# Optimization experiments

Measured on AMD Instinct MI355X. Metric: run time of the kernel, lower is better.

The kernel has to match this reference:

```python
import jax, jax.numpy as jnp
import numpy as np

N = 50000
E = 1_600_000
IN_C = 128
OUT_C = 128


def _glorot(key, shape):
    fan_in, fan_out = shape[0], shape[1]
    s = jnp.sqrt(6.0 / (fan_in + fan_out))
    return jax.random.uniform(key, shape, jnp.float32, -s, s)


def setup_inputs() -> dict:
    key = jax.random.key(0)
    ks = jax.random.split(key, 32)
    inp = {
        'X': jax.random.normal(ks[0], (N, IN_C), jnp.float32),
        'edge_index': jax.random.randint(ks[1], (2, E), 0, N, jnp.int64),
        'edge_weight': jax.random.uniform(ks[2], (E,), jnp.float32),
        'H': jax.random.normal(ks[3], (N, OUT_C), jnp.float32),
        'C': jax.random.normal(ks[4], (N, OUT_C), jnp.float32),
    }
    i = 5
    for g in ('i', 'f', 'c', 'o'):
        inp[f'Wx_{g}'] = _glorot(ks[i], (IN_C, OUT_C)); i += 1
        inp[f'bx_{g}'] = jnp.zeros((OUT_C,), jnp.float32)
        inp[f'Wh_{g}'] = _glorot(ks[i], (OUT_C, OUT_C)); i += 1
        inp[f'bh_{g}'] = jnp.zeros((OUT_C,), jnp.float32)
    for g in ('i', 'f', 'o'):
        inp[f'w_c_{g}'] = _glorot(ks[i], (1, OUT_C)); i += 1
    for g in ('i', 'f', 'c', 'o'):
        inp[f'b_{g}'] = jnp.zeros((1, OUT_C), jnp.float32)
    return inp


def reference(X, edge_index, edge_weight, H, C,
              Wx_i, bx_i, Wh_i, bh_i,
              Wx_f, bx_f, Wh_f, bh_f,
              Wx_c, bx_c, Wh_c, bh_c,
              Wx_o, bx_o, Wh_o, bh_o,
              w_c_i, w_c_f, w_c_o,
              b_i, b_f, b_c, b_o):
    n = X.shape[0]
    src, dst = edge_index[0], edge_index[1]
    # GCN normalization (add_self_loops=False): deg from destination (in-degree)
    deg = jax.ops.segment_sum(edge_weight, dst, num_segments=n)
    dis = jnp.where(deg > 0, jax.lax.rsqrt(jnp.where(deg > 0, deg, 1.0)), 0.0)
    norm = dis[src] * edge_weight * dis[dst]  # [E]

    def gcn(x, W, b):
        xw = x @ W                       # [n, OUT_C]
        msg = xw[src] * norm[:, None]    # gather + scale, [E, OUT_C]
        return jax.ops.segment_sum(msg, dst, num_segments=n) + b

    I = jax.nn.sigmoid(gcn(X, Wx_i, bx_i) + gcn(H, Wh_i, bh_i) + w_c_i * C + b_i)
    Fg = jax.nn.sigmoid(gcn(X, Wx_f, bx_f) + gcn(H, Wh_f, bh_f) + w_c_f * C + b_f)
    T = jnp.tanh(gcn(X, Wx_c, bx_c) + gcn(H, Wh_c, bh_c) + b_c)
    Cn = Fg * C + I * T
    O = jax.nn.sigmoid(gcn(X, Wx_o, bx_o) + gcn(H, Wh_o, bh_o) + w_c_o * Cn + b_o)
    Hn = O * jnp.tanh(Cn)
    return Hn, Cn
```

## Files before the change

### kernel.cpp

```cpp
#include <hip/hip_runtime.h>

__device__ __forceinline__ float bf2f(unsigned short u){
    union { unsigned int i; float f; } v; v.i = ((unsigned int)u) << 16; return v.f;
}
__device__ __forceinline__ unsigned short f2bf(float f){
    union { unsigned int i; float f; } v; v.f = f;
    unsigned int i = v.i;
    unsigned int r = i + 0x7FFFu + ((i >> 16) & 1u);
    return (unsigned short)(r >> 16);
}
__device__ __forceinline__ float sigm(float x){ return 1.0f / (1.0f + __expf(-x)); }

__device__ __forceinline__ float ldsel(const void* p, size_t idx, int fF){
    float r;
    if (fF) r = ((const float*)p)[idx];
    else    r = bf2f(((const unsigned short*)p)[idx]);
    return r;
}

typedef __attribute__((ext_vector_type(8))) short s8v;
typedef __attribute__((ext_vector_type(4))) float f4v;

__global__ void k_detect(const unsigned short* __restrict__ X,
                         const int* __restrict__ ei, int* __restrict__ flags){
    __shared__ int cnt, nz;
    if (threadIdx.x == 0){ cnt = 0; nz = 0; }
    __syncthreads();
    int ok = 0;
    for (int i = threadIdx.x; i < 2048; i += 256){
        int e = (X[i] >> 7) & 0xFF;
        if (e >= 96 && e <= 160) ok++;
    }
    atomicAdd(&cnt, ok);
    int nzl = 0;
    for (int i = threadIdx.x; i < 128; i += 256)
        if (ei[2*i + 1] != 0) nzl++;
    atomicAdd(&nz, nzl);
    __syncthreads();
    if (threadIdx.x == 0){
        flags[0] = (cnt < 1843) ? 1 : 0;
        flags[1] = (nz == 0)   ? 1 : 0;
    }
}

struct PackArgs {
    const void* Wx[4];
    const void* Wh[4];
    const void* bx[4];
    const void* bh[4];
};

__global__ void k_tobf(const void* __restrict__ X, const void* __restrict__ H,
                       uint4* __restrict__ XHb128, const int* __restrict__ flags,
                       int N){
    int t = blockIdx.x*256 + threadIdx.x;
    if (t >= N*32) return;
    int n = t >> 5, i = t & 31;
    int fF = flags[0];
    int q = (i < 16) ? i : i - 16;
    uint4 o;
    if (fF){
        const float4* src = (const float4*)((i < 16) ? X : H);
        float4 a = src[(size_t)n*32 + q*2];
        float4 b = src[(size_t)n*32 + q*2 + 1];
        o.x = ((unsigned int)f2bf(a.y) << 16) | f2bf(a.x);
        o.y = ((unsigned int)f2bf(a.w) << 16) | f2bf(a.z);
        o.z = ((unsigned int)f2bf(b.y) << 16) | f2bf(b.x);
        o.w = ((unsigned int)f2bf(b.w) << 16) | f2bf(b.z);
    } else {
        const uint4* src = (const uint4*)((i < 16) ? X : H);
        o = src[(size_t)n*16 + q];
    }
    XHb128[(size_t)n*32 + i] = o;
}

__global__ void k_cnt(const int* __restrict__ ei, int* __restrict__ cnt,
                      int* __restrict__ off, const int* __restrict__ flags,
                      int E, int N){
    int base = blockIdx.x*1024 + threadIdx.x;
    int fI = flags[1];
#pragma unroll
    for (int k = 0; k < 4; k++){
        int e = base + k*256;
        if (e >= E) break;
        int d = fI ? ei[2*(size_t)E + 2*(size_t)e] : ei[(size_t)E + e];
        if ((unsigned)d >= (unsigned)N) continue;
        off[e] = atomicAdd(&cnt[d], 1);
    }
}

__global__ void k_pack(PackArgs pa, unsigned short* __restrict__ Bp,
                       float* __restrict__ bias, const int* __restrict__ flags){
    int t = blockIdx.x*256 + threadIdx.x;
    int fF = flags[0];
    {
        int j    =  t        & 7;
        int lane = (t >> 3)  & 63;
        int kb   = (t >> 9)  & 7;
        int ct   = (t >> 12) & 7;
        int g    = (t >> 15) & 3;
        int k   = kb*32 + (lane >> 4)*8 + j;
        int col = ct*16 + (lane & 15);
        const void* p; size_t idx;
        if (k < 128){ p = pa.Wx[g]; idx = (size_t)k*128 + col; }
        else        { p = pa.Wh[g]; idx = (size_t)(k-128)*128 + col; }
        unsigned short v;
        if (fF) v = f2bf(((const float*)p)[idx]);
        else    v = ((const unsigned short*)p)[idx];
        Bp[t] = v;
    }
    if (t < 512){
        int g = t >> 7, c = t & 127;
        bias[t] = ldsel(pa.bx[g], c, fF) + ldsel(pa.bh[g], c, fF);
    }
}

__global__ void k_scanA(const int* __restrict__ cnt, int* __restrict__ bsum, int n){
    __shared__ int sh[256];
    int t = threadIdx.x, i = blockIdx.x * 256 + t;
    sh[t] = (i < n) ? cnt[i] : 0;
    __syncthreads();
    for (int o = 128; o > 0; o >>= 1){
        if (t < o) sh[t] += sh[t + o];
        __syncthreads();
    }
    if (t == 0) bsum[blockIdx.x] = sh[0];
}
__global__ void k_scanB(const int* __restrict__ bsum, int* __restrict__ bsumoff, int nb){
    __shared__ int sh[256];
    int t = threadIdx.x;
    int v = (t < nb) ? bsum[t] : 0;
    sh[t] = v;
    __syncthreads();
    for (int o = 1; o < 256; o <<= 1){
        int u = (t >= o) ? sh[t - o] : 0;
        __syncthreads();
        sh[t] += u;
        __syncthreads();
    }
    bsumoff[t] = sh[t] - v;
}
__global__ void k_scanC(const int* __restrict__ cnt, const int* __restrict__ bsumoff,
                        int* __restrict__ rowstart, int n){
    __shared__ int sh[256];
    int t = threadIdx.x, i = blockIdx.x * 256 + t;
    int v = (i < n) ? cnt[i] : 0;
    sh[t] = v;
    __syncthreads();
    for (int o = 1; o < 256; o <<= 1){
        int u = (t >= o) ? sh[t - o] : 0;
        __syncthreads();
        sh[t] += u;
        __syncthreads();
    }
    int incl = sh[t];
    if (i < n)     rowstart[i] = bsumoff[blockIdx.x] + incl - v;
    if (i == n-1)  rowstart[n] = bsumoff[blockIdx.x] + incl;
}

__global__ void k_scatter(const int* __restrict__ ei, const void* __restrict__ ew,
                          const int* __restrict__ rowstart, const int* __restrict__ off,
                          int2* __restrict__ recs, const int* __restrict__ flags,
                          int E, int N){
    int base = blockIdx.x*512 + threadIdx.x;
    int fF = flags[0], fI = flags[1];
#pragma unroll
    for (int k = 0; k < 2; k++){
        int e = base + k*256;
        if (e >= E) break;
        int s, d;
        if (fI){ s = ei[2*(size_t)e]; d = ei[2*(size_t)E + 2*(size_t)e]; }
        else   { s = ei[e];           d = ei[(size_t)E + e]; }
        if ((unsigned)d >= (unsigned)N) continue;
        float w = 0.f; int ss = 0;
        if ((unsigned)s < (unsigned)N){ w = ldsel(ew, e, fF); ss = s; }
        int2 r; r.x = ss; r.y = __float_as_int(w);
        recs[rowstart[d] + off[e]] = r;
    }
}

__global__ __launch_bounds__(256)
void k_degdis(const int2* __restrict__ recs, const int* __restrict__ rowstart,
              float* __restrict__ dis, int N){
    int gw = (blockIdx.x * 256 + threadIdx.x) >> 6;
    int lane = threadIdx.x & 63;
    if (gw >= N) return;
    int beg = rowstart[gw], end = rowstart[gw + 1];
    float sw = 0.f;
    for (int i = beg + lane; i < end; i += 64) sw += __int_as_float(recs[i].y);
    for (int o = 32; o > 0; o >>= 1) sw += __shfl_down(sw, o);
    if (lane == 0) dis[gw] = (sw > 0.f) ? rsqrtf(sw) : 0.f;
}

__global__ __launch_bounds__(256)
void k_gather(const int2* __restrict__ recs, const int* __restrict__ rowstart,
              const float* __restrict__ dis, const uint4* __restrict__ XHb128,
              uint4* __restrict__ AXH128, int N){
    int node = (blockIdx.x * 256 + threadIdx.x) >> 6;
    int lane = threadIdx.x & 63;
    if (node >= N) return;
    int half = lane >> 5;
    int sub  = lane & 31;
    int beg = rowstart[node], end = rowstart[node + 1];
    float disd = dis[node];
    float a0=0.f,a1=0.f,a2=0.f,a3=0.f,a4=0.f,a5=0.f,a6=0.f,a7=0.f;

#define ACC8(v, n)                                              \
    a0 += (n) * bf2f((unsigned short)((v).x & 0xffff));         \
    a1 += (n) * bf2f((unsigned short)((v).x >> 16));            \
    a2 += (n) * bf2f((unsigned short)((v).y & 0xffff));         \
    a3 += (n) * bf2f((unsigned short)((v).y >> 16));            \
    a4 += (n) * bf2f((unsigned short)((v).z & 0xffff));         \
    a5 += (n) * bf2f((unsigned short)((v).z >> 16));            \
    a6 += (n) * bf2f((unsigned short)((v).w & 0xffff));         \
    a7 += (n) * bf2f((unsigned short)((v).w >> 16));

    int i = beg;
    for (; i + 3 < end; i += 4){
        int2 rA = recs[i + half];
        int2 rB = recs[i + 2 + half];
        uint4 vA = XHb128[(size_t)rA.x*32 + sub];
        uint4 vB = XHb128[(size_t)rB.x*32 + sub];
        float nA = dis[rA.x] * __int_as_float(rA.y) * disd;
        float nB = dis[rB.x] * __int_as_float(rB.y) * disd;
        ACC8(vA, nA);
        ACC8(vB, nB);
    }
    if (end - i >= 2){
        int2 rA = recs[i + half];
        uint4 vA = XHb128[(size_t)rA.x*32 + sub];
        float nA = dis[rA.x] * __int_as_float(rA.y) * disd;
        ACC8(vA, nA);
        i += 2;
    }
    if (i < end){
        int2 rA = recs[i];
        uint4 vA = XHb128[(size_t)rA.x*32 + sub];
        float nA = (half == 0) ? dis[rA.x] * __int_as_float(rA.y) * disd : 0.f;
        ACC8(vA, nA);
    }
#undef ACC8

    a0 += __shfl_xor(a0, 32, 64);
    a1 += __shfl_xor(a1, 32, 64);
    a2 += __shfl_xor(a2, 32, 64);
    a3 += __shfl_xor(a3, 32, 64);
    a4 += __shfl_xor(a4, 32, 64);
    a5 += __shfl_xor(a5, 32, 64);
    a6 += __shfl_xor(a6, 32, 64);
    a7 += __shfl_xor(a7, 32, 64);

    if (half == 0){
        uint4 o;
        o.x = ((unsigned int)f2bf(a1) << 16) | f2bf(a0);
        o.y = ((unsigned int)f2bf(a3) << 16) | f2bf(a2);
        o.z = ((unsigned int)f2bf(a5) << 16) | f2bf(a4);
        o.w = ((unsigned int)f2bf(a7) << 16) | f2bf(a6);
        AXH128[(size_t)node*32 + sub] = o;
    }
}

struct EpiArgs {
    const void *C, *wci, *wcf, *wco, *bi, *bff, *bc, *bo;
};

__global__ __launch_bounds__(256)
void k_gemm(const unsigned short* __restrict__ AXH,
            const unsigned short* __restrict__ Bp, const float* __restrict__ bias,
            EpiArgs ea, void* __restrict__ outp, const int* __restrict__ flags, int N){
    int tid  = threadIdx.x;
    int w    = tid >> 6, lane = tid & 63;
    int node0 = blockIdx.x * 32;
    int fF = flags[0];

    f4v acc[2][8];
#pragma unroll
    for (int m = 0; m < 2; m++)
#pragma unroll
        for (int c = 0; c < 8; c++) acc[m][c] = (f4v){0.f,0.f,0.f,0.f};

    const unsigned short* a0base = AXH + (size_t)(node0 + (lane & 15))*256 + (lane >> 4)*8;
    const unsigned short* a1base = a0base + 16*256;
#pragma unroll
    for (int kb = 0; kb < 8; kb++){
        s8v af0 = *(const s8v*)(a0base + kb*32);
        s8v af1 = *(const s8v*)(a1base + kb*32);
#pragma unroll
        for (int ct8 = 0; ct8 < 8; ct8++){
            int g = ct8 >> 1, sub = ct8 & 1;
            const s8v bfrag = *(const s8v*)(Bp + g*32768 + (size_t)(w*2 + sub)*4096
                                            + kb*512 + lane*8);
            acc[0][ct8] = __builtin_amdgcn_mfma_f32_16x16x32_bf16(af0, bfrag, acc[0][ct8], 0, 0, 0);
            acc[1][ct8] = __builtin_amdgcn_mfma_f32_16x16x32_bf16(af1, bfrag, acc[1][ct8], 0, 0, 0);
        }
    }

    int q = lane >> 4, cl = lane & 15;
#pragma unroll
    for (int sub = 0; sub < 2; sub++){
        int c = w*32 + sub*16 + cl;
        float bvi = bias[0*128 + c], bvf = bias[1*128 + c];
        float bvc = bias[2*128 + c], bvo = bias[3*128 + c];
        float wci = ldsel(ea.wci, c, fF), wcf = ldsel(ea.wcf, c, fF), wco = ldsel(ea.wco, c, fF);
        float bi  = ldsel(ea.bi, c, fF),  bff = ldsel(ea.bff, c, fF);
        float bc  = ldsel(ea.bc, c, fF),  bo  = ldsel(ea.bo, c, fF);
#pragma unroll
        for (int m = 0; m < 2; m++){
#pragma unroll
            for (int r = 0; r < 4; r++){
                int node = node0 + m*16 + q*4 + r;
                if (node >= N) continue;
                size_t gidx = (size_t)node*128 + c;
                float Cv = ldsel(ea.C, gidx, fF);
                float pi  = acc[m][0+sub][r] + bvi;
                float pf  = acc[m][2+sub][r] + bvf;
                float pcv = acc[m][4+sub][r] + bvc;
                float po  = acc[m][6+sub][r] + bvo;
                float Iv = sigm(pi + wci*Cv + bi);
                float Fv = sigm(pf + wcf*Cv + bff);
                float Tv = tanhf(pcv + bc);
                float Cn = Fv*Cv + Iv*Tv;
                float Ov = sigm(po + wco*Cn + bo);
                float Hn = Ov * tanhf(Cn);
                if (fF){
                    ((float*)outp)[gidx] = Hn;
                    ((float*)outp)[(size_t)N*128 + gidx] = Cn;
                } else {
                    ((unsigned short*)outp)[gidx] = f2bf(Hn);
                    ((unsigned short*)outp)[(size_t)N*128 + gidx] = f2bf(Cn);
                }
            }
        }
    }
}

extern "C" void kernel_launch(void* const* d_in, const int* in_sizes, int n_in,
                              void* d_out, int out_size, void* d_ws, size_t ws_size,
                              hipStream_t stream){
    const void* X  = d_in[0];
    const int*  ei = (const int*)d_in[1];
    const void* ew = d_in[2];
    const void* H  = d_in[3];
    const void* C  = d_in[4];
    const int N = in_sizes[0] / 128;
    const int E = in_sizes[2];

    char* ws = (char*)d_ws;
    int*   cnt          = (int*)  (ws);
    float* dis          = (float*)(ws + ((size_t)256 << 10));
    int*   rowstart     = (int*)  (ws + ((size_t)512 << 10));
    int*   bsum         = (int*)  (ws + ((size_t)768 << 10));
    int*   bsumoff      = (int*)  (ws + ((size_t)772 << 10));
    int*   flags        = (int*)  (ws + ((size_t)776 << 10));
    unsigned short* Bp  = (unsigned short*)(ws + ((size_t)1 << 20));
    float* bias         = (float*)(ws + ((size_t)1 << 20) + ((size_t)256 << 10));
    int*   off          = (int*)  (ws + ((size_t)2 << 20));
    unsigned int* AXH32 = (unsigned int*)(ws + ((size_t)2 << 20));
    int2*  recs         = (int2*) (ws + ((size_t)28 << 20));
    unsigned int* XHb32 = (unsigned int*)(ws + ((size_t)41 << 20));

    hipMemsetAsync(cnt, 0, (size_t)256 << 10, stream);
    k_detect<<<1, 256, 0, stream>>>((const unsigned short*)X, ei, flags);

    PackArgs pa;
    pa.Wx[0]=d_in[5];  pa.bx[0]=d_in[6];  pa.Wh[0]=d_in[7];  pa.bh[0]=d_in[8];
    pa.Wx[1]=d_in[9];  pa.bx[1]=d_in[10]; pa.Wh[1]=d_in[11]; pa.bh[1]=d_in[12];
    pa.Wx[2]=d_in[13]; pa.bx[2]=d_in[14]; pa.Wh[2]=d_in[15]; pa.bh[2]=d_in[16];
    pa.Wx[3]=d_in[17]; pa.bx[3]=d_in[18]; pa.Wh[3]=d_in[19]; pa.bh[3]=d_in[20];

    k_cnt<<<(E + 1023)/1024, 256, 0, stream>>>(ei, cnt, off, flags, E, N);
    k_tobf<<<(N*32 + 255)/256, 256, 0, stream>>>(X, H, (uint4*)XHb32, flags, N);
    k_pack<<<512, 256, 0, stream>>>(pa, Bp, bias, flags);

    int nbA = (N + 255)/256;
    k_scanA<<<nbA, 256, 0, stream>>>(cnt, bsum, N);
    k_scanB<<<1, 256, 0, stream>>>(bsum, bsumoff, nbA);
    k_scanC<<<nbA, 256, 0, stream>>>(cnt, bsumoff, rowstart, N);

    k_scatter<<<(E + 511)/512, 256, 0, stream>>>(ei, ew, rowstart, off, recs, flags, E, N);
    k_degdis<<<(N*64 + 255)/256, 256, 0, stream>>>(recs, rowstart, dis, N);
    k_gather<<<(N*64 + 255)/256, 256, 0, stream>>>(recs, rowstart, dis,
                                                   (const uint4*)XHb32,
                                                   (uint4*)AXH32, N);

    EpiArgs ea;
    ea.C   = C;
    ea.wci = d_in[21];
    ea.wcf = d_in[22];
    ea.wco = d_in[23];
    ea.bi  = d_in[24];
    ea.bff = d_in[25];
    ea.bc  = d_in[26];
    ea.bo  = d_in[27];
    k_gemm<<<(N + 31)/32, 256, 0, stream>>>((const unsigned short*)AXH32, Bp, bias,
                                            ea, d_out, flags, N);
}
```

Before: 506.2 us.

## Fuse preprocessing kernels, compute degree with atomics, unroll gather deeper

The edge-count, bf16 conversion and weight-packing kernels are merged into one launch that branches on block index. The weighted in-degree is now accumulated with float atomics during counting, and the inverse square root is folded into the scan. That removes the separate per-node degree-reduction pass over the edge records. The scatter kernel batches four edges' loads per thread before storing, and the gather loop is unrolled to eight edges to keep more loads in flight. The trade-offs are extra float atomic traffic, a summation order that is no longer deterministic, and higher register pressure in the gather kernel.

```diff
diff --git a/kernel.cpp b/kernel.cpp
--- a/kernel.cpp
+++ b/kernel.cpp
@@ -50,68 +50,79 @@
     const void* bh[4];
 };
 
-__global__ void k_tobf(const void* __restrict__ X, const void* __restrict__ H,
-                       uint4* __restrict__ XHb128, const int* __restrict__ flags,
-                       int N){
-    int t = blockIdx.x*256 + threadIdx.x;
-    if (t >= N*32) return;
-    int n = t >> 5, i = t & 31;
+__global__ void k_fused1(const void* __restrict__ X, const void* __restrict__ H,
+                         uint4* __restrict__ XHb128,
+                         const int* __restrict__ ei, const void* __restrict__ ew,
+                         int* __restrict__ cnt, float* __restrict__ deg,
+                         int* __restrict__ off,
+                         PackArgs pa, unsigned short* __restrict__ Bp,
+                         float* __restrict__ bias,
+                         const int* __restrict__ flags,
+                         int nbC, int nbT, int E, int N){
+    int b = blockIdx.x;
     int fF = flags[0];
-    int q = (i < 16) ? i : i - 16;
-    uint4 o;
-    if (fF){
-        const float4* src = (const float4*)((i < 16) ? X : H);
-        float4 a = src[(size_t)n*32 + q*2];
-        float4 b = src[(size_t)n*32 + q*2 + 1];
-        o.x = ((unsigned int)f2bf(a.y) << 16) | f2bf(a.x);
-        o.y = ((unsigned int)f2bf(a.w) << 16) | f2bf(a.z);
-        o.z = ((unsigned int)f2bf(b.y) << 16) | f2bf(b.x);
-        o.w = ((unsigned int)f2bf(b.w) << 16) | f2bf(b.z);
+    if (b < nbC){
+        int base = b*2048 + threadIdx.x;
+        int fI = flags[1];
+        int dd[8]; float wv[8];
+#pragma unroll
+        for (int k = 0; k < 8; k++){
+            int e = base + k*256;
+            dd[k] = -1; wv[k] = 0.f;
+            if (e < E){
+                dd[k] = fI ? ei[2*(size_t)E + 2*(size_t)e] : ei[(size_t)E + e];
+                wv[k] = ldsel(ew, e, fF);
+            }
+        }
+#pragma unroll
+        for (int k = 0; k < 8; k++){
+            int e = base + k*256;
+            if (e < E && (unsigned)dd[k] < (unsigned)N){
+                off[e] = atomicAdd(&cnt[dd[k]], 1);
+                atomicAdd(&deg[dd[k]], wv[k]);
+            }
+        }
+    } else if (b < nbC + nbT){
+        int t = (b - nbC)*256 + threadIdx.x;
+        if (t >= N*32) return;
+        int n = t >> 5, i = t & 31;
+        int q = (i < 16) ? i : i - 16;
+        uint4 o;
+        if (fF){
+            const float4* src = (const float4*)((i < 16) ? X : H);
+            float4 a = src[(size_t)n*32 + q*2];
+            float4 bb = src[(size_t)n*32 + q*2 + 1];
+            o.x = ((unsigned int)f2bf(a.y) << 16) | f2bf(a.x);
+            o.y = ((unsigned int)f2bf(a.w) << 16) | f2bf(a.z);
+            o.z = ((unsigned int)f2bf(bb.y) << 16) | f2bf(bb.x);
+            o.w = ((unsigned int)f2bf(bb.w) << 16) | f2bf(bb.z);
+        } else {
+            const uint4* src = (const uint4*)((i < 16) ? X : H);
+            o = src[(size_t)n*16 + q];
+        }
+        XHb128[(size_t)n*32 + i] = o;
     } else {
-        const uint4* src = (const uint4*)((i < 16) ? X : H);
-        o = src[(size_t)n*16 + q];
-    }
-    XHb128[(size_t)n*32 + i] = o;
-}
-
-__global__ void k_cnt(const int* __restrict__ ei, int* __restrict__ cnt,
-                      int* __restrict__ off, const int* __restrict__ flags,
-                      int E, int N){
-    int base = blockIdx.x*1024 + threadIdx.x;
-    int fI = flags[1];
-#pragma unroll
-    for (int k = 0; k < 4; k++){
-        int e = base + k*256;
-        if (e >= E) break;
-        int d = fI ? ei[2*(size_t)E + 2*(size_t)e] : ei[(size_t)E + e];
-        if ((unsigned)d >= (unsigned)N) continue;
-        off[e] = atomicAdd(&cnt[d], 1);
-    }
-}
-
-__global__ void k_pack(PackArgs pa, unsigned short* __restrict__ Bp,
-                       float* __restrict__ bias, const int* __restrict__ flags){
-    int t = blockIdx.x*256 + threadIdx.x;
-    int fF = flags[0];
-    {
-        int j    =  t        & 7;
-        int lane = (t >> 3)  & 63;
-        int kb   = (t >> 9)  & 7;
-        int ct   = (t >> 12) & 7;
-        int g    = (t >> 15) & 3;
-        int k   = kb*32 + (lane >> 4)*8 + j;
-        int col = ct*16 + (lane & 15);
-        const void* p; size_t idx;
-        if (k < 128){ p = pa.Wx[g]; idx = (size_t)k*128 + col; }
-        else        { p = pa.Wh[g]; idx = (size_t)(k-128)*128 + col; }
-        unsigned short v;
-        if (fF) v = f2bf(((const float*)p)[idx]);
-        else    v = ((const unsigned short*)p)[idx];
-        Bp[t] = v;
-    }
-    if (t < 512){
-        int g = t >> 7, c = t & 127;
-        bias[t] = ldsel(pa.bx[g], c, fF) + ldsel(pa.bh[g], c, fF);
+        int t = (b - nbC - nbT)*256 + threadIdx.x;
+        if (t < 4*8*8*64*8){
+            int j    =  t        & 7;
+            int lane = (t >> 3)  & 63;
+            int kb   = (t >> 9)  & 7;
+            int ct   = (t >> 12) & 7;
+            int g    = (t >> 15) & 3;
+            int k   = kb*32 + (lane >> 4)*8 + j;
+            int col = ct*16 + (lane & 15);
+            const void* p; size_t idx;
+            if (k < 128){ p = pa.Wx[g]; idx = (size_t)k*128 + col; }
+            else        { p = pa.Wh[g]; idx = (size_t)(k-128)*128 + col; }
+            unsigned short v;
+            if (fF) v = f2bf(((const float*)p)[idx]);
+            else    v = ((const unsigned short*)p)[idx];
+            Bp[t] = v;
+        }
+        if (t < 512){
+            int g = t >> 7, c = t & 127;
+            bias[t] = ldsel(pa.bx[g], c, fF) + ldsel(pa.bh[g], c, fF);
+        }
     }
 }
 
@@ -141,7 +152,8 @@
     bsumoff[t] = sh[t] - v;
 }
 __global__ void k_scanC(const int* __restrict__ cnt, const int* __restrict__ bsumoff,
-                        int* __restrict__ rowstart, int n){
+                        const float* __restrict__ deg,
+                        int* __restrict__ rowstart, float* __restrict__ dis, int n){
     __shared__ int sh[256];
     int t = threadIdx.x, i = blockIdx.x * 256 + t;
     int v = (i < n) ? cnt[i] : 0;
@@ -154,7 +166,11 @@
         __syncthreads();
     }
     int incl = sh[t];
-    if (i < n)     rowstart[i] = bsumoff[blockIdx.x] + incl - v;
+    if (i < n){
+        rowstart[i] = bsumoff[blockIdx.x] + incl - v;
+        float dg = deg[i];
+        dis[i] = (dg > 0.f) ? rsqrtf(dg) : 0.f;
+    }
     if (i == n-1)  rowstart[n] = bsumoff[blockIdx.x] + incl;
 }
 
@@ -162,34 +178,28 @@
                           const int* __restrict__ rowstart, const int* __restrict__ off,
                           int2* __restrict__ recs, const int* __restrict__ flags,
                           int E, int N){
-    int base = blockIdx.x*512 + threadIdx.x;
+    int base = blockIdx.x*1024 + threadIdx.x;
     int fF = flags[0], fI = flags[1];
-#pragma unroll
-    for (int k = 0; k < 2; k++){
+    int ss[4], dd[4], oo[4]; float wv[4];
+#pragma unroll
+    for (int k = 0; k < 4; k++){
         int e = base + k*256;
-        if (e >= E) break;
-        int s, d;
-        if (fI){ s = ei[2*(size_t)e]; d = ei[2*(size_t)E + 2*(size_t)e]; }
-        else   { s = ei[e];           d = ei[(size_t)E + e]; }
-        if ((unsigned)d >= (unsigned)N) continue;
-        float w = 0.f; int ss = 0;
-        if ((unsigned)s < (unsigned)N){ w = ldsel(ew, e, fF); ss = s; }
-        int2 r; r.x = ss; r.y = __float_as_int(w);
-        recs[rowstart[d] + off[e]] = r;
-    }
-}
-
-__global__ __launch_bounds__(256)
-void k_degdis(const int2* __restrict__ recs, const int* __restrict__ rowstart,
-              float* __restrict__ dis, int N){
-    int gw = (blockIdx.x * 256 + threadIdx.x) >> 6;
-    int lane = threadIdx.x & 63;
-    if (gw >= N) return;
-    int beg = rowstart[gw], end = rowstart[gw + 1];
-    float sw = 0.f;
-    for (int i = beg + lane; i < end; i += 64) sw += __int_as_float(recs[i].y);
-    for (int o = 32; o > 0; o >>= 1) sw += __shfl_down(sw, o);
-    if (lane == 0) dis[gw] = (sw > 0.f) ? rsqrtf(sw) : 0.f;
+        dd[k] = -1; ss[k] = 0; wv[k] = 0.f; oo[k] = 0;
+        if (e < E){
+            if (fI){ ss[k] = ei[2*(size_t)e]; dd[k] = ei[2*(size_t)E + 2*(size_t)e]; }
+            else   { ss[k] = ei[e];           dd[k] = ei[(size_t)E + e]; }
+            oo[k] = off[e];
+            if ((unsigned)ss[k] < (unsigned)N) wv[k] = ldsel(ew, e, fF);
+            else ss[k] = 0;
+        }
+    }
+#pragma unroll
+    for (int k = 0; k < 4; k++){
+        if ((unsigned)dd[k] < (unsigned)N){
+            int2 r; r.x = ss[k]; r.y = __float_as_int(wv[k]);
+            recs[rowstart[dd[k]] + oo[k]] = r;
+        }
+    }
 }
 
 __global__ __launch_bounds__(256)
@@ -216,22 +226,29 @@
     a7 += (n) * bf2f((unsigned short)((v).w >> 16));
 
     int i = beg;
-    for (; i + 3 < end; i += 4){
-        int2 rA = recs[i + half];
+    for (; i + 7 < end; i += 8){
+        int2 rA = recs[i     + half];
         int2 rB = recs[i + 2 + half];
+        int2 rC = recs[i + 4 + half];
+        int2 rD = recs[i + 6 + half];
         uint4 vA = XHb128[(size_t)rA.x*32 + sub];
         uint4 vB = XHb128[(size_t)rB.x*32 + sub];
+        uint4 vC = XHb128[(size_t)rC.x*32 + sub];
+        uint4 vD = XHb128[(size_t)rD.x*32 + sub];
         float nA = dis[rA.x] * __int_as_float(rA.y) * disd;
         float nB = dis[rB.x] * __int_as_float(rB.y) * disd;
+        float nC = dis[rC.x] * __int_as_float(rC.y) * disd;
+        float nD = dis[rD.x] * __int_as_float(rD.y) * disd;
         ACC8(vA, nA);
         ACC8(vB, nB);
-    }
-    if (end - i >= 2){
+        ACC8(vC, nC);
+        ACC8(vD, nD);
+    }
+    for (; i + 1 < end; i += 2){
         int2 rA = recs[i + half];
         uint4 vA = XHb128[(size_t)rA.x*32 + sub];
         float nA = dis[rA.x] * __int_as_float(rA.y) * disd;
         ACC8(vA, nA);
-        i += 2;
     }
     if (i < end){
         int2 rA = recs[i];
@@ -347,11 +364,12 @@
 
     char* ws = (char*)d_ws;
     int*   cnt          = (int*)  (ws);
-    float* dis          = (float*)(ws + ((size_t)256 << 10));
+    float* deg          = (float*)(ws + ((size_t)256 << 10));
     int*   rowstart     = (int*)  (ws + ((size_t)512 << 10));
     int*   bsum         = (int*)  (ws + ((size_t)768 << 10));
     int*   bsumoff      = (int*)  (ws + ((size_t)772 << 10));
     int*   flags        = (int*)  (ws + ((size_t)776 << 10));
+    float* dis          = (float*)(ws + ((size_t)780 << 10));
     unsigned short* Bp  = (unsigned short*)(ws + ((size_t)1 << 20));
     float* bias         = (float*)(ws + ((size_t)1 << 20) + ((size_t)256 << 10));
     int*   off          = (int*)  (ws + ((size_t)2 << 20));
@@ -359,7 +377,7 @@
     int2*  recs         = (int2*) (ws + ((size_t)28 << 20));
     unsigned int* XHb32 = (unsigned int*)(ws + ((size_t)41 << 20));
 
-    hipMemsetAsync(cnt, 0, (size_t)256 << 10, stream);
+    hipMemsetAsync(cnt, 0, (size_t)512 << 10, stream);
     k_detect<<<1, 256, 0, stream>>>((const unsigned short*)X, ei, flags);
 
     PackArgs pa;
@@ -368,17 +386,18 @@
     pa.Wx[2]=d_in[13]; pa.bx[2]=d_in[14]; pa.Wh[2]=d_in[15]; pa.bh[2]=d_in[16];
     pa.Wx[3]=d_in[17]; pa.bx[3]=d_in[18]; pa.Wh[3]=d_in[19]; pa.bh[3]=d_in[20];
 
-    k_cnt<<<(E + 1023)/1024, 256, 0, stream>>>(ei, cnt, off, flags, E, N);
-    k_tobf<<<(N*32 + 255)/256, 256, 0, stream>>>(X, H, (uint4*)XHb32, flags, N);
-    k_pack<<<512, 256, 0, stream>>>(pa, Bp, bias, flags);
+    int nbC = (E + 2047)/2048;
+    int nbT = (N*32 + 255)/256;
+    k_fused1<<<nbC + nbT + 512, 256, 0, stream>>>(X, H, (uint4*)XHb32, ei, ew,
+                                                  cnt, deg, off, pa, Bp, bias,
+                                                  flags, nbC, nbT, E, N);
 
     int nbA = (N + 255)/256;
     k_scanA<<<nbA, 256, 0, stream>>>(cnt, bsum, N);
     k_scanB<<<1, 256, 0, stream>>>(bsum, bsumoff, nbA);
-    k_scanC<<<nbA, 256, 0, stream>>>(cnt, bsumoff, rowstart, N);
-
-    k_scatter<<<(E + 511)/512, 256, 0, stream>>>(ei, ew, rowstart, off, recs, flags, E, N);
-    k_degdis<<<(N*64 + 255)/256, 256, 0, stream>>>(recs, rowstart, dis, N);
+    k_scanC<<<nbA, 256, 0, stream>>>(cnt, bsumoff, deg, rowstart, dis, N);
+
+    k_scatter<<<(E + 1023)/1024, 256, 0, stream>>>(ei, ew, rowstart, off, recs, flags, E, N);
     k_gather<<<(N*64 + 255)/256, 256, 0, stream>>>(recs, rowstart, dis,
                                                    (const uint4*)XHb32,
                                                    (uint4*)AXH32, N);
```

Measured after the change: 550.7 us. 8.8% more time.
